# Kernel optimization log

Hardware: AMD Instinct MI355X
Metric: run time of the kernel (lower is better)

Reference implementation:

```python
import jax, jax.numpy as jnp
import numpy as np
from jax import lax

N, C, H, W = 8, 512, 28, 28
G = 8                     # attention groups
QKP = 32                  # qk_planes = out/groups/2
VP = 64                   # v_planes = branch/groups
BP = 512                  # branch_planes
HW = H * W
EPS = 1e-5                # BatchNorm eps (eval mode, running_mean=0, running_var=1)


def bn(x, gamma, beta, axis=1):
    shape = [1] * x.ndim
    shape[axis] = x.shape[axis]
    g = gamma.reshape(shape)
    b = beta.reshape(shape)
    return x * (g / jnp.sqrt(1.0 + EPS)) + b


def conv2d(x, w, groups=1):
    return lax.conv_general_dilated(
        x, w, (1, 1), 'SAME',
        dimension_numbers=('NCHW', 'OIHW', 'NCHW'),
        feature_group_count=groups)


def setup_inputs() -> dict:
    key = jax.random.key(0)
    ks = jax.random.split(key, 16)
    pe_dim = 2 * QKP + VP  # 128
    inp = {
        'x':        jax.random.normal(ks[0], (N, C, H, W), jnp.float32),
        'qkv_w':    jax.random.normal(ks[1], (BP * 2, C), jnp.float32) * np.sqrt(1.0 / C),
        'g_qkv':    jax.random.normal(ks[2], (BP * 2,), jnp.float32) * 0.1 + 1.0,
        'b_qkv':    jax.random.normal(ks[3], (BP * 2,), jnp.float32) * 0.1,
        'g_sim':    jax.random.normal(ks[4], (G * 3,), jnp.float32) * 0.1 + 1.0,
        'b_sim':    jax.random.normal(ks[5], (G * 3,), jnp.float32) * 0.1,
        'g_out':    jax.random.normal(ks[6], (BP * 2,), jnp.float32) * 0.1 + 1.0,
        'b_out':    jax.random.normal(ks[7], (BP * 2,), jnp.float32) * 0.1,
        'relative': jax.random.normal(ks[8], (pe_dim, 2 * HW - 1), jnp.float32) * np.sqrt(1.0 / VP),
        'xw1':      jax.random.normal(ks[9], (BP, C // G, 3, 3), jnp.float32) * np.sqrt(2.0 / (C // G * 9)),
        'xw2':      jax.random.normal(ks[10], (BP, BP, 1, 1), jnp.float32) * np.sqrt(2.0 / BP),
        'g_x':      jnp.ones((BP,), jnp.float32),
        'b_x':      jnp.zeros((BP,), jnp.float32),
        'rw':       jax.random.normal(ks[11], (BP, BP * 2, 1, 1), jnp.float32) * np.sqrt(2.0 / (BP * 2)),
        'g_r':      jnp.ones((BP,), jnp.float32),
        'b_r':      jnp.zeros((BP,), jnp.float32),
        'pw':       jax.random.normal(ks[12], (BP, BP, 1, 1), jnp.float32) * np.sqrt(2.0 / BP),
        'g_p':      jnp.ones((BP,), jnp.float32),
        'b_p':      jnp.zeros((BP,), jnp.float32),
    }
    return inp


def reference(x, qkv_w, g_qkv, b_qkv, g_sim, b_sim, g_out, b_out, relative,
              xw1, xw2, g_x, b_x, rw, g_r, b_r, pw, g_p, b_p):
    n = x.shape[0]
    # ---- unary branch: grouped 3x3 conv + 1x1 conv + BN ----
    unary = conv2d(x, xw1, groups=G)
    unary = conv2d(unary, xw2)
    unary = bn(unary, g_x, b_x)

    # ---- binary branch (attention over HW tokens) ----
    xf = x.reshape(n, C, HW)
    qkv = jnp.einsum('oc,bci->boi', qkv_w, xf)          # Conv1d k=1
    qkv = bn(qkv, g_qkv, b_qkv)
    qkv = qkv.reshape(n, G, 2 * QKP + VP, HW)
    q = qkv[:, :, :QKP]
    k = qkv[:, :, QKP:2 * QKP]
    v = qkv[:, :, 2 * QKP:]

    # relative position embeddings via index gather: emb[c,i,j] = relative[c, i-j+HW-1]
    idx = jnp.arange(HW)
    rel_idx = idx[:, None] - idx[None, :] + HW - 1      # [HW, HW]
    emb = relative[:, rel_idx]                           # [pe_dim, HW, HW]
    q_emb, k_emb, v_emb = emb[:QKP], emb[QKP:2 * QKP], emb[2 * QKP:]

    qk = jnp.einsum('bgci,bgcj->bgij', q, k)
    qr = jnp.einsum('bgci,cij->bgij', q, q_emb)
    kr = jnp.einsum('bgci,cij->bgij', k, k_emb).swapaxes(2, 3)
    stacked = jnp.concatenate([qk, qr, kr], axis=1)      # [n, 3G, HW, HW]
    stacked = bn(stacked, g_sim, b_sim)
    logits = stacked.reshape(n, 3, G, HW, HW).sum(axis=1)
    sim = jax.nn.softmax(logits, axis=-1)                # softmax over keys j

    sv = jnp.einsum('bgij,bgcj->bgci', sim, v)
    sve = jnp.einsum('bgij,cij->bgci', sim, v_emb)
    stacked_binary = jnp.concatenate([sv, sve], axis=-1).reshape(n, BP * 2, HW)
    stacked_binary = bn(stacked_binary, g_out, b_out)
    binary = stacked_binary.reshape(n, BP, 2, HW).sum(axis=2).reshape(n, BP, H, W)

    # ---- gating / reasoning path ----
    gate_in = jnp.concatenate([unary, binary], axis=1)   # [n, 2*BP, H, W]
    r = jax.nn.relu(gate_in)
    r = jax.nn.relu(bn(conv2d(r, rw), g_r, b_r))
    gate = jax.nn.sigmoid(bn(conv2d(r, pw), g_p, b_p))

    return gate * binary + unary


if __name__ == '__main__':
    out = reference(**setup_inputs())
    print(out.shape, out.dtype)
```

## Files before the change

kernel.cpp:

```cpp
#include <hip/hip_runtime.h>
#include <math.h>


typedef unsigned short u16;
typedef unsigned int u32;
typedef __bf16 bf16x8 __attribute__((ext_vector_type(8)));
typedef float f32x4 __attribute__((ext_vector_type(4)));

#define INVS 0.99999500003749968f
#define MFMA16(a, b, c) __builtin_amdgcn_mfma_f32_16x16x32_bf16(a, b, c, 0, 0, 0)

__device__ inline u16 f2bf(float f) {
  u32 u = __builtin_bit_cast(u32, f);
  return (u16)((u + 0x7fffu + ((u >> 16) & 1u)) >> 16);
}
__device__ inline bf16x8 ld_bf8(const u16* p) {
  int4 v = *reinterpret_cast<const int4*>(p);
  return __builtin_bit_cast(bf16x8, v);
}
__device__ inline bf16x8 pack8(const u16 h[8]) {
  int4 v;
  v.x = (int)((u32)h[0] | ((u32)h[1] << 16));
  v.y = (int)((u32)h[2] | ((u32)h[3] << 16));
  v.z = (int)((u32)h[4] | ((u32)h[5] << 16));
  v.w = (int)((u32)h[6] | ((u32)h[7] << 16));
  return __builtin_bit_cast(bf16x8, v);
}
__device__ inline bf16x8 zero8() {
  int4 z = {0, 0, 0, 0};
  return __builtin_bit_cast(bf16x8, z);
}
__device__ inline float bpermf(float v, int srcl) {
  return __builtin_bit_cast(float,
      __builtin_amdgcn_ds_bpermute(srcl << 2, __builtin_bit_cast(int, v)));
}

__global__ __launch_bounds__(256) void k_prep(
    const float* __restrict__ qkv_w, const float* __restrict__ xw2,
    const float* __restrict__ rw, const float* __restrict__ pw,
    const float* __restrict__ xw1, const float* __restrict__ rel,
    u16* __restrict__ Wq, u16* __restrict__ W2, u16* __restrict__ Wr,
    u16* __restrict__ Wp, u16* __restrict__ W1t, u16* __restrict__ relq,
    u16* __restrict__ relk, u16* __restrict__ relv) {
  int idx = blockIdx.x * 256 + threadIdx.x;
  if (idx < 524288) { Wq[idx] = f2bf(qkv_w[idx]); return; }
  idx -= 524288;
  if (idx < 262144) { W2[idx] = f2bf(xw2[idx]); return; }
  idx -= 262144;
  if (idx < 524288) { Wr[idx] = f2bf(rw[idx]); return; }
  idx -= 524288;
  if (idx < 262144) { Wp[idx] = f2bf(pw[idx]); return; }
  idx -= 262144;
  if (idx < 294912) {
    int gk = idx >> 12, rem = idx & 4095, oc = rem >> 6, ic = rem & 63;
    int g = gk / 9, k9 = gk % 9;
    W1t[idx] = f2bf(xw1[(((g * 64 + oc) * 64) + ic) * 9 + k9]);
    return;
  }
  idx -= 294912;
  if (idx < 51200) {
    int t = idx >> 5, c = idx & 31;
    relq[idx] = (t < 1567) ? f2bf(rel[c * 1567 + t]) : (u16)0;
    return;
  }
  idx -= 51200;
  if (idx < 51200) {
    int t = idx >> 5, c = idx & 31;
    relk[idx] = (t < 1567) ? f2bf(rel[(32 + c) * 1567 + t]) : (u16)0;
    return;
  }
  idx -= 51200;
  if (idx < 102400) {
    int c = idx / 1600, t = idx % 1600;
    relv[idx] = (t < 1567) ? f2bf(rel[(64 + c) * 1567 + t]) : (u16)0;
    return;
  }
}

__global__ __launch_bounds__(256) void k_transpose(const float* __restrict__ x,
                                                   u16* __restrict__ xT) {
  const int b = blockIdx.z, c0 = blockIdx.y * 64, n0 = blockIdx.x * 32;
  const int tid = threadIdx.x;
  __shared__ __align__(16) u16 tl[64][36];
#pragma unroll
  for (int h = 0; h < 2; ++h) {
    int cl = (tid >> 3) + h * 32;
    int n4 = (tid & 7) * 4;
    float4 v = {0.f, 0.f, 0.f, 0.f};
    if (n0 + n4 + 3 < 784)
      v = *reinterpret_cast<const float4*>(x + ((size_t)b * 512 + c0 + cl) * 784 + n0 + n4);
    u32 lo = (u32)f2bf(v.x) | ((u32)f2bf(v.y) << 16);
    u32 hi = (u32)f2bf(v.z) | ((u32)f2bf(v.w) << 16);
    *reinterpret_cast<int2*>(&tl[cl][n4]) = make_int2((int)lo, (int)hi);
  }
  __syncthreads();
  int nl = tid >> 3, c8 = (tid & 7) * 8;
  if (n0 + nl < 784) {
    u16 h[8];
#pragma unroll
    for (int e = 0; e < 8; ++e) h[e] = tl[c8 + e][nl];
    *reinterpret_cast<int4*>(xT + ((size_t)b * 784 + n0 + nl) * 512 + c0 + c8) =
        __builtin_bit_cast(int4, pack8(h));
  }
}

__global__ __launch_bounds__(256) void k_gemm_qkv(
    const u16* __restrict__ W, const u16* __restrict__ xT,
    const float* __restrict__ gq, const float* __restrict__ bq,
    u16* __restrict__ Qs, u16* __restrict__ Ks, u16* __restrict__ Vs) {
  const int b = blockIdx.z, mt = blockIdx.y, n0 = blockIdx.x * 112;
  const int tid = threadIdx.x, lane = tid & 63, wave = tid >> 6;
  const int lm = lane & 15, lq = lane >> 4;
  __shared__ __align__(16) u16 Bl[112 * 40];
  f32x4 zf = {0.f, 0.f, 0.f, 0.f};
  f32x4 acc[7];
#pragma unroll
  for (int t = 0; t < 7; ++t) acc[t] = zf;
  const u16* Bb = xT + ((size_t)b * 784 + n0) * 512;
  const u16* Ar = W + (size_t)(mt * 64 + wave * 16 + lm) * 512;
  const int row0 = tid >> 2, seg8 = (tid & 3) * 8;
  const u16* src0 = Bb + (size_t)row0 * 512 + seg8;
  const u16* src1 = src0 + (size_t)64 * 512;
  u16* dst0 = &Bl[row0 * 40 + seg8];
  u16* dst1 = &Bl[(row0 + 64) * 40 + seg8];
  int4 p0 = *reinterpret_cast<const int4*>(src0);
  int4 p1;
  if (tid < 192) p1 = *reinterpret_cast<const int4*>(src1);
  bf16x8 afc = ld_bf8(Ar + lq * 8);
  for (int ks = 0; ks < 16; ++ks) {
    *reinterpret_cast<int4*>(dst0) = p0;
    if (tid < 192) *reinterpret_cast<int4*>(dst1) = p1;
    __syncthreads();
    bf16x8 af = afc;
    if (ks < 15) {
      p0 = *reinterpret_cast<const int4*>(src0 + (ks + 1) * 32);
      if (tid < 192) p1 = *reinterpret_cast<const int4*>(src1 + (ks + 1) * 32);
      afc = ld_bf8(Ar + (ks + 1) * 32 + lq * 8);
    }
#pragma unroll
    for (int t = 0; t < 7; ++t) {
      bf16x8 bf8 = ld_bf8(&Bl[(t * 16 + lm) * 40 + lq * 8]);
      acc[t] = MFMA16(af, bf8, acc[t]);
    }
    __syncthreads();
  }
  const int og = mt * 64 + wave * 16 + lq * 4;
  float sc[4], bi[4];
#pragma unroll
  for (int r = 0; r < 4; ++r) { sc[r] = gq[og + r] * INVS; bi[r] = bq[og + r]; }
  const int g = og >> 7, r128 = og & 127;
  const size_t bg = (size_t)b * 8 + g;
#pragma unroll
  for (int t = 0; t < 7; ++t) {
    int j = n0 + t * 16 + lm;
    u16 h[4];
#pragma unroll
    for (int r = 0; r < 4; ++r) h[r] = f2bf(acc[t][r] * sc[r] + bi[r]);
    if (r128 < 64) {
      u16* dst = (r128 < 32) ? Qs : Ks;
      int c = r128 & 31;
      u32 lo = (u32)h[0] | ((u32)h[1] << 16);
      u32 hi = (u32)h[2] | ((u32)h[3] << 16);
      *reinterpret_cast<int2*>(dst + (bg * 784 + j) * 32 + c) = make_int2((int)lo, (int)hi);
    } else {
      int c = r128 - 64;
#pragma unroll
      for (int r = 0; r < 4; ++r) Vs[(bg * 64 + c + r) * 784 + j] = h[r];
    }
  }
}

__global__ __launch_bounds__(256) void k_conv1(const u16* __restrict__ xT,
                                               const u16* __restrict__ W1t,
                                               u16* __restrict__ umid) {
  const int b = blockIdx.z, g = blockIdx.y, n0 = blockIdx.x * 112;
  const int tid = threadIdx.x, lane = tid & 63, wave = tid >> 6;
  const int lm = lane & 15, lq = lane >> 4;
  __shared__ __align__(16) u16 xl[170 * 72];
  for (int u = tid; u < 1360; u += 256) {
    int row = u >> 3, seg = u & 7;
    int ng = n0 - 29 + row;
    int4 v = {0, 0, 0, 0};
    if (ng >= 0 && ng < 784)
      v = *reinterpret_cast<const int4*>(xT + ((size_t)b * 784 + ng) * 512 + g * 64 + seg * 8);
    *reinterpret_cast<int4*>(&xl[row * 72 + seg * 8]) = v;
  }
  __syncthreads();
  f32x4 zf = {0.f, 0.f, 0.f, 0.f};
  f32x4 acc[7];
#pragma unroll
  for (int t = 0; t < 7; ++t) acc[t] = zf;
  const u16* Wg = W1t + (size_t)g * 9 * 4096;
#pragma unroll
  for (int k9 = 0; k9 < 9; ++k9) {
    const int dh = k9 / 3 - 1, dw = k9 % 3 - 1;
#pragma unroll
    for (int ks = 0; ks < 2; ++ks) {
      bf16x8 af = ld_bf8(Wg + (k9 * 64 + wave * 16 + lm) * 64 + ks * 32 + lq * 8);
#pragma unroll
      for (int t = 0; t < 7; ++t) {
        int n = n0 + t * 16 + lm;
        int ww = n % 28 + dw;
        bf16x8 bf8;
        if (ww >= 0 && ww < 28)
          bf8 = ld_bf8(&xl[(t * 16 + lm + dh * 28 + dw + 29) * 72 + ks * 32 + lq * 8]);
        else
          bf8 = zero8();
        acc[t] = MFMA16(af, bf8, acc[t]);
      }
    }
  }
  const int oc4 = g * 64 + wave * 16 + lq * 4;
#pragma unroll
  for (int t = 0; t < 7; ++t) {
    int j = n0 + t * 16 + lm;
    u16 h[4];
#pragma unroll
    for (int r = 0; r < 4; ++r) h[r] = f2bf(acc[t][r]);
    u32 lo = (u32)h[0] | ((u32)h[1] << 16);
    u32 hi = (u32)h[2] | ((u32)h[3] << 16);
    *reinterpret_cast<int2*>(umid + ((size_t)b * 784 + j) * 512 + oc4) = make_int2((int)lo, (int)hi);
  }
}

__global__ __launch_bounds__(256) void k_gemm_x2(
    const u16* __restrict__ W, const u16* __restrict__ Bsrc,
    const float* __restrict__ gv, const float* __restrict__ bv,
    float* __restrict__ outT) {
  const int b = blockIdx.z, mt = blockIdx.y, n0 = blockIdx.x * 112;
  const int tid = threadIdx.x, lane = tid & 63, wave = tid >> 6;
  const int lm = lane & 15, lq = lane >> 4;
  __shared__ __align__(16) u16 Bl[112 * 40];
  f32x4 zf = {0.f, 0.f, 0.f, 0.f};
  f32x4 acc[7];
#pragma unroll
  for (int t = 0; t < 7; ++t) acc[t] = zf;
  const u16* Bb = Bsrc + ((size_t)b * 784 + n0) * 512;
  const u16* Ar = W + (size_t)(mt * 64 + wave * 16 + lm) * 512;
  const int row0 = tid >> 2, seg8 = (tid & 3) * 8;
  const u16* src0 = Bb + (size_t)row0 * 512 + seg8;
  const u16* src1 = src0 + (size_t)64 * 512;
  u16* dst0 = &Bl[row0 * 40 + seg8];
  u16* dst1 = &Bl[(row0 + 64) * 40 + seg8];
  int4 p0 = *reinterpret_cast<const int4*>(src0);
  int4 p1;
  if (tid < 192) p1 = *reinterpret_cast<const int4*>(src1);
  bf16x8 afc = ld_bf8(Ar + lq * 8);
  for (int ks = 0; ks < 16; ++ks) {
    *reinterpret_cast<int4*>(dst0) = p0;
    if (tid < 192) *reinterpret_cast<int4*>(dst1) = p1;
    __syncthreads();
    bf16x8 af = afc;
    if (ks < 15) {
      p0 = *reinterpret_cast<const int4*>(src0 + (ks + 1) * 32);
      if (tid < 192) p1 = *reinterpret_cast<const int4*>(src1 + (ks + 1) * 32);
      afc = ld_bf8(Ar + (ks + 1) * 32 + lq * 8);
    }
#pragma unroll
    for (int t = 0; t < 7; ++t) {
      bf16x8 bf8 = ld_bf8(&Bl[(t * 16 + lm) * 40 + lq * 8]);
      acc[t] = MFMA16(af, bf8, acc[t]);
    }
    __syncthreads();
  }
  const int og = mt * 64 + wave * 16 + lq * 4;
  float sc[4], bi[4];
#pragma unroll
  for (int r = 0; r < 4; ++r) { sc[r] = gv[og + r] * INVS; bi[r] = bv[og + r]; }
#pragma unroll
  for (int t = 0; t < 7; ++t) {
    int j = n0 + t * 16 + lm;
    float4 o4;
    o4.x = acc[t][0] * sc[0] + bi[0];
    o4.y = acc[t][1] * sc[1] + bi[1];
    o4.z = acc[t][2] * sc[2] + bi[2];
    o4.w = acc[t][3] * sc[3] + bi[3];
    *reinterpret_cast<float4*>(outT + ((size_t)b * 784 + j) * 512 + og) = o4;
  }
}

__global__ __launch_bounds__(256) void k_attn(
    const u16* __restrict__ Qs, const u16* __restrict__ Ks, const u16* __restrict__ Vs,
    const u16* __restrict__ relq, const u16* __restrict__ relk, const u16* __restrict__ relv,
    const float* __restrict__ g_sim, const float* __restrict__ g_out,
    const float* __restrict__ b_out, float* __restrict__ binT) {
  const int b = blockIdx.z, g = blockIdx.y, i0 = blockIdx.x * 16;
  const int tid = threadIdx.x, lane = tid & 63, wave = tid >> 6;
  const int lm = lane & 15, lq = lane >> 4;
  __shared__ __align__(16) u16 Pl[16 + 16 * 872];
  __shared__ __align__(16) float KRs[4][16][34];
  __shared__ float WM[4][16];
  __shared__ float rstat[16];
  for (int u = tid; u < 1424; u += 256) {
    int idx = (u < 16) ? u : (16 + ((u - 16) / 88) * 872 + 784 + (u - 16) % 88);
    Pl[idx] = 0;
  }
  const float s0 = g_sim[g] * INVS, s1 = g_sim[8 + g] * INVS, s2 = g_sim[16 + g] * INVS;
  const size_t bg = (size_t)b * 8 + g;
  const u16* Qb = Qs + bg * 784 * 32;
  const u16* Kb = Ks + bg * 784 * 32;
  const u16* Vb = Vs + bg * 64 * 784;
  const bf16x8 aq = ld_bf8(Qb + (i0 + lm) * 32 + lq * 8);
  const f32x4 zf = {0.f, 0.f, 0.f, 0.f};
  float vmax[4] = {-1e30f, -1e30f, -1e30f, -1e30f};
  bf16x8 kfc, bq0c, bq1c, bk0c, bk1c;
  {
    const int j0 = wave * 16;
    const int d0 = 768 + i0 - j0, e0 = 768 + j0 - i0;
    kfc = ld_bf8(Kb + (j0 + lm) * 32 + lq * 8);
    bq0c = ld_bf8(relq + (d0 + lm) * 32 + lq * 8);
    bq1c = ld_bf8(relq + (d0 + 16 + lm) * 32 + lq * 8);
    bk0c = ld_bf8(relk + (e0 + lm) * 32 + lq * 8);
    bk1c = ld_bf8(relk + (e0 + 16 + lm) * 32 + lq * 8);
  }
  int jt = wave;
  for (int rr = 0; rr < 13; ++rr) {
    const int jtn = jt + 4;
    bf16x8 kfn = kfc, bq0n = bq0c, bq1n = bq1c, bk0n = bk0c, bk1n = bk1c;
    if (jtn < 49) {
      const int j0n = jtn * 16;
      const int d0 = 768 + i0 - j0n, e0 = 768 + j0n - i0;
      kfn = ld_bf8(Kb + (j0n + lm) * 32 + lq * 8);
      bq0n = ld_bf8(relq + (d0 + lm) * 32 + lq * 8);
      bq1n = ld_bf8(relq + (d0 + 16 + lm) * 32 + lq * 8);
      bk0n = ld_bf8(relk + (e0 + lm) * 32 + lq * 8);
      bk1n = ld_bf8(relk + (e0 + 16 + lm) * 32 + lq * 8);
    }
    if (jt < 49) {
      const int j0 = jt * 16;
      f32x4 aqk = MFMA16(aq, kfc, zf);
      f32x4 q0 = MFMA16(aq, bq0c, zf);
      f32x4 q1 = MFMA16(aq, bq1c, zf);
      f32x4 k0 = MFMA16(kfc, bk0c, zf);
      f32x4 k1 = MFMA16(kfc, bk1c, zf);
#pragma unroll
      for (int r = 0; r < 4; ++r) {
        int m = lq * 4 + r;
        KRs[wave][m][lm] = k0[r];
        KRs[wave][m][16 + lm] = k1[r];
      }
#pragma unroll
      for (int r = 0; r < 4; ++r) {
        int m = lq * 4 + r, n = lm;
        int c = m - n + 15;
        int srcl = (c & 15) | (lane & 48);
        float t0 = bpermf(q0[r], srcl), t1 = bpermf(q1[r], srcl);
        float qv = (c & 16) ? t1 : t0;
        float kv = KRs[wave][n][n - m + 15];
        float val = aqk[r] * s0 + qv * s1 + kv * s2;
        vmax[r] = fmaxf(vmax[r], val);
        _Float16 hv = (_Float16)val;
        Pl[16 + m * 872 + j0 + n] = __builtin_bit_cast(u16, hv);
      }
    }
    jt = jtn;
    kfc = kfn; bq0c = bq0n; bq1c = bq1n; bk0c = bk0n; bk1c = bk1n;
  }
#pragma unroll
  for (int r = 0; r < 4; ++r) {
#pragma unroll
    for (int d = 1; d < 16; d <<= 1) vmax[r] = fmaxf(vmax[r], __shfl_xor(vmax[r], d, 64));
  }
  if (lm == 0) {
#pragma unroll
    for (int r = 0; r < 4; ++r) WM[wave][lq * 4 + r] = vmax[r];
  }
  __syncthreads();
  {
    const int row = tid >> 4, sub = tid & 15;
    u16* Pr = &Pl[16 + row * 872];
    float gmax = fmaxf(fmaxf(WM[0][row], WM[1][row]), fmaxf(WM[2][row], WM[3][row]));
    float sm = 0.f;
    for (int k = 0; k < 49; ++k) {
      int j = sub + 16 * k;
      _Float16 hv = __builtin_bit_cast(_Float16, Pr[j]);
      float e = __expf((float)hv - gmax);
      sm += e;
      Pr[j] = f2bf(e);
    }
#pragma unroll
    for (int d = 1; d < 16; d <<= 1) sm += __shfl_xor(sm, d, 64);
    if (sub == 0) rstat[row] = 1.0f / sm;
  }
  __syncthreads();
  f32x4 accV = zf, accE = zf;
  const int coff = wave * 16;
  const u16* Vr = Vb + (size_t)(coff + lm) * 784;
  const u16* Rr = relv + (size_t)(coff + lm) * 1600 + i0;
  const u16* Prow = &Pl[16 + lm * 872];
  for (int ks = 0; ks < 25; ++ks) {
    bf16x8 ap = ld_bf8(Prow + ks * 32 + lq * 8);
    bf16x8 bv = ld_bf8(Vr + ks * 32 + lq * 8);
    accV = MFMA16(ap, bv, accV);
    const int base = 783 + lm - ks * 32 - lq * 8;
    u16 h[8];
#pragma unroll
    for (int e = 0; e < 8; ++e) h[e] = Prow[base - e];
    bf16x8 ash = pack8(h);
    bf16x8 br = ld_bf8(Rr + ks * 32 + lq * 8);
    accE = MFMA16(ash, br, accE);
  }
  const int c = coff + lm;
  const int oi = g * 128 + 2 * c;
  const float so0 = g_out[oi] * INVS, bo0 = b_out[oi];
  const float so1 = g_out[oi + 1] * INVS, bo1 = b_out[oi + 1];
#pragma unroll
  for (int r = 0; r < 4; ++r) {
    int row = lq * 4 + r;
    float rl = rstat[row];
    float val = accV[r] * rl * so0 + bo0 + accE[r] * rl * so1 + bo1;
    binT[((size_t)b * 784 + i0 + row) * 512 + g * 64 + c] = val;
  }
}

__global__ __launch_bounds__(256) void k_gemm_rw(
    const u16* __restrict__ W, const float* __restrict__ unT, const float* __restrict__ binT,
    const float* __restrict__ gv, const float* __restrict__ bv, u16* __restrict__ rT) {
  const int b = blockIdx.z, mt = blockIdx.y, n0 = blockIdx.x * 112;
  const int tid = threadIdx.x, lane = tid & 63, wave = tid >> 6;
  const int lm = lane & 15, lq = lane >> 4;
  __shared__ __align__(16) u16 Bl[112 * 40];
  f32x4 zf = {0.f, 0.f, 0.f, 0.f};
  f32x4 acc[7];
#pragma unroll
  for (int t = 0; t < 7; ++t) acc[t] = zf;
  const u16* Ar = W + (size_t)(mt * 64 + wave * 16 + lm) * 1024;
  const int row0 = tid >> 2, seg8 = (tid & 3) * 8;
  const size_t off0 = ((size_t)b * 784 + n0 + row0) * 512 + seg8;
  const size_t off1 = off0 + (size_t)64 * 512;
  u16* dst0 = &Bl[row0 * 40 + seg8];
  u16* dst1 = &Bl[(row0 + 64) * 40 + seg8];
  auto ldrow = [](const float* sp, float4& a, float4& b) {
    a = *reinterpret_cast<const float4*>(sp);
    b = *reinterpret_cast<const float4*>(sp + 4);
  };
  auto cvt_store = [](u16* dst, float4 a, float4 b) {
    u16 h[8] = {f2bf(fmaxf(a.x, 0.f)), f2bf(fmaxf(a.y, 0.f)),
                f2bf(fmaxf(a.z, 0.f)), f2bf(fmaxf(a.w, 0.f)),
                f2bf(fmaxf(b.x, 0.f)), f2bf(fmaxf(b.y, 0.f)),
                f2bf(fmaxf(b.z, 0.f)), f2bf(fmaxf(b.w, 0.f))};
    *reinterpret_cast<int4*>(dst) = __builtin_bit_cast(int4, pack8(h));
  };
  float4 a0, b0, a1, b1;
  ldrow(unT + off0, a0, b0);
  if (tid < 192) ldrow(unT + off1, a1, b1);
  bf16x8 afc = ld_bf8(Ar + lq * 8);
  for (int ks = 0; ks < 32; ++ks) {
    cvt_store(dst0, a0, b0);
    if (tid < 192) cvt_store(dst1, a1, b1);
    __syncthreads();
    bf16x8 af = afc;
    if (ks < 31) {
      const int ksn = ks + 1;
      const float* sb = (ksn < 16) ? unT : binT;
      const int k0 = (ksn & 15) * 32;
      ldrow(sb + off0 + k0, a0, b0);
      if (tid < 192) ldrow(sb + off1 + k0, a1, b1);
      afc = ld_bf8(Ar + ksn * 32 + lq * 8);
    }
#pragma unroll
    for (int t = 0; t < 7; ++t) {
      bf16x8 bf8 = ld_bf8(&Bl[(t * 16 + lm) * 40 + lq * 8]);
      acc[t] = MFMA16(af, bf8, acc[t]);
    }
    __syncthreads();
  }
  const int og = mt * 64 + wave * 16 + lq * 4;
  float sc[4], bi[4];
#pragma unroll
  for (int r = 0; r < 4; ++r) { sc[r] = gv[og + r] * INVS; bi[r] = bv[og + r]; }
#pragma unroll
  for (int t = 0; t < 7; ++t) {
    int j = n0 + t * 16 + lm;
    u16 h[4];
#pragma unroll
    for (int r = 0; r < 4; ++r) h[r] = f2bf(fmaxf(acc[t][r] * sc[r] + bi[r], 0.f));
    u32 lo = (u32)h[0] | ((u32)h[1] << 16);
    u32 hi = (u32)h[2] | ((u32)h[3] << 16);
    *reinterpret_cast<int2*>(rT + ((size_t)b * 784 + j) * 512 + og) = make_int2((int)lo, (int)hi);
  }
}

__global__ __launch_bounds__(256) void k_gemm_pw(
    const u16* __restrict__ W, const u16* __restrict__ rT,
    const float* __restrict__ gv, const float* __restrict__ bv,
    const float* __restrict__ binT, const float* __restrict__ unT,
    float* __restrict__ out) {
  const int b = blockIdx.z, mt = blockIdx.y, n0 = blockIdx.x * 112;
  const int tid = threadIdx.x, lane = tid & 63, wave = tid >> 6;
  const int lm = lane & 15, lq = lane >> 4;
  __shared__ __align__(16) u16 Bl[112 * 40];
  f32x4 zf = {0.f, 0.f, 0.f, 0.f};
  f32x4 acc[7];
#pragma unroll
  for (int t = 0; t < 7; ++t) acc[t] = zf;
  const u16* Bb = rT + ((size_t)b * 784 + n0) * 512;
  const u16* Ar = W + (size_t)(mt * 64 + wave * 16 + lm) * 512;
  const int row0 = tid >> 2, seg8 = (tid & 3) * 8;
  const u16* src0 = Bb + (size_t)row0 * 512 + seg8;
  const u16* src1 = src0 + (size_t)64 * 512;
  u16* dst0 = &Bl[row0 * 40 + seg8];
  u16* dst1 = &Bl[(row0 + 64) * 40 + seg8];
  int4 p0 = *reinterpret_cast<const int4*>(src0);
  int4 p1;
  if (tid < 192) p1 = *reinterpret_cast<const int4*>(src1);
  bf16x8 afc = ld_bf8(Ar + lq * 8);
  for (int ks = 0; ks < 16; ++ks) {
    *reinterpret_cast<int4*>(dst0) = p0;
    if (tid < 192) *reinterpret_cast<int4*>(dst1) = p1;
    __syncthreads();
    bf16x8 af = afc;
    if (ks < 15) {
      p0 = *reinterpret_cast<const int4*>(src0 + (ks + 1) * 32);
      if (tid < 192) p1 = *reinterpret_cast<const int4*>(src1 + (ks + 1) * 32);
      afc = ld_bf8(Ar + (ks + 1) * 32 + lq * 8);
    }
#pragma unroll
    for (int t = 0; t < 7; ++t) {
      bf16x8 bf8 = ld_bf8(&Bl[(t * 16 + lm) * 40 + lq * 8]);
      acc[t] = MFMA16(af, bf8, acc[t]);
    }
    __syncthreads();
  }
  const int og = mt * 64 + wave * 16 + lq * 4;
  float sc[4], bi[4];
#pragma unroll
  for (int r = 0; r < 4; ++r) { sc[r] = gv[og + r] * INVS; bi[r] = bv[og + r]; }
#pragma unroll
  for (int t = 0; t < 7; ++t) {
    int j = n0 + t * 16 + lm;
    float4 bin4 = *reinterpret_cast<const float4*>(binT + ((size_t)b * 784 + j) * 512 + og);
    float4 un4 = *reinterpret_cast<const float4*>(unT + ((size_t)b * 784 + j) * 512 + og);
    float binv[4] = {bin4.x, bin4.y, bin4.z, bin4.w};
    float unv[4] = {un4.x, un4.y, un4.z, un4.w};
#pragma unroll
    for (int r = 0; r < 4; ++r) {
      float gt = 1.f / (1.f + __expf(-(acc[t][r] * sc[r] + bi[r])));
      out[((size_t)b * 512 + og + r) * 784 + j] = gt * binv[r] + unv[r];
    }
  }
}

extern "C" void kernel_launch(void* const* d_in, const int* in_sizes, int n_in,
                              void* d_out, int out_size, void* d_ws, size_t ws_size,
                              hipStream_t stream) {
  const float* x = (const float*)d_in[0];
  const float* qkv_w = (const float*)d_in[1];
  const float* g_qkv = (const float*)d_in[2];
  const float* b_qkv = (const float*)d_in[3];
  const float* g_sim = (const float*)d_in[4];
  const float* g_out = (const float*)d_in[6];
  const float* b_out = (const float*)d_in[7];
  const float* relative = (const float*)d_in[8];
  const float* xw1 = (const float*)d_in[9];
  const float* xw2 = (const float*)d_in[10];
  const float* g_x = (const float*)d_in[11];
  const float* b_x = (const float*)d_in[12];
  const float* rw = (const float*)d_in[13];
  const float* g_r = (const float*)d_in[14];
  const float* b_r = (const float*)d_in[15];
  const float* pw = (const float*)d_in[16];
  const float* g_p = (const float*)d_in[17];
  const float* b_p = (const float*)d_in[18];

  char* p = (char*)d_ws;
  auto take = [&](size_t n) { char* q = p; p += (n + 255) & ~(size_t)255; return q; };
  u16* xT = (u16*)take((size_t)8 * 784 * 512 * 2);
  u16* Wq = (u16*)take((size_t)1024 * 512 * 2);
  u16* W2 = (u16*)take((size_t)512 * 512 * 2);
  u16* Wr = (u16*)take((size_t)512 * 1024 * 2);
  u16* Wp = (u16*)take((size_t)512 * 512 * 2);
  u16* W1t = (u16*)take((size_t)294912 * 2);
  u16* relq = (u16*)take((size_t)51200 * 2);
  u16* relk = (u16*)take((size_t)51200 * 2);
  u16* relv = (u16*)take((size_t)102400 * 2);
  u16* Qs = (u16*)take((size_t)8 * 8 * 784 * 32 * 2);
  u16* Ks = (u16*)take((size_t)8 * 8 * 784 * 32 * 2);
  u16* Vs = (u16*)take(((size_t)8 * 8 * 64 * 784 + 64) * 2);
  u16* umid = (u16*)take((size_t)8 * 784 * 512 * 2);
  float* unT = (float*)take((size_t)8 * 784 * 512 * 4);
  float* binT = (float*)take((size_t)8 * 784 * 512 * 4);
  u16* rT = (u16*)take((size_t)8 * 784 * 512 * 2);

  k_prep<<<dim3(8096), dim3(256), 0, stream>>>(qkv_w, xw2, rw, pw, xw1, relative,
                                               Wq, W2, Wr, Wp, W1t, relq, relk, relv);
  k_transpose<<<dim3(25, 8, 8), dim3(256), 0, stream>>>(x, xT);
  k_gemm_qkv<<<dim3(7, 16, 8), dim3(256), 0, stream>>>(Wq, xT, g_qkv, b_qkv, Qs, Ks, Vs);
  k_conv1<<<dim3(7, 8, 8), dim3(256), 0, stream>>>(xT, W1t, umid);
  k_gemm_x2<<<dim3(7, 8, 8), dim3(256), 0, stream>>>(W2, umid, g_x, b_x, unT);
  k_attn<<<dim3(49, 8, 8), dim3(256), 0, stream>>>(Qs, Ks, Vs, relq, relk, relv,
                                                   g_sim, g_out, b_out, binT);
  k_gemm_rw<<<dim3(7, 8, 8), dim3(256), 0, stream>>>(Wr, unT, binT, g_r, b_r, rT);
  k_gemm_pw<<<dim3(7, 8, 8), dim3(256), 0, stream>>>(Wp, rT, g_p, b_p, binT, unT,
                                                     (float*)d_out);
}
```

Measured before the change: 301.0 us.

## Merge independent kernels into combined launches with block-index dispatch

Independent stages are paired into single launches: transpose with weight prep, conv1 with the QKV GEMM, and the x2 GEMM with attention. Each pair shares a flat grid, and the block index selects which body runs. This cuts the kernel count from eight to five and lets independent work fill the GPU together, reducing launch gaps and tail idle time. The cost is that each merged kernel's shared memory is sized for the larger body (up to about 37KB), which may lower occupancy for the lighter blocks.

```diff
diff --git a/kernel.cpp b/kernel.cpp
--- a/kernel.cpp
+++ b/kernel.cpp
@@ -35,14 +35,14 @@
       __builtin_amdgcn_ds_bpermute(srcl << 2, __builtin_bit_cast(int, v)));
 }
 
-__global__ __launch_bounds__(256) void k_prep(
-    const float* __restrict__ qkv_w, const float* __restrict__ xw2,
+
+__device__ void body_prep(
+    int idx, const float* __restrict__ qkv_w, const float* __restrict__ xw2,
     const float* __restrict__ rw, const float* __restrict__ pw,
     const float* __restrict__ xw1, const float* __restrict__ rel,
     u16* __restrict__ Wq, u16* __restrict__ W2, u16* __restrict__ Wr,
     u16* __restrict__ Wp, u16* __restrict__ W1t, u16* __restrict__ relq,
     u16* __restrict__ relk, u16* __restrict__ relv) {
-  int idx = blockIdx.x * 256 + threadIdx.x;
   if (idx < 524288) { Wq[idx] = f2bf(qkv_w[idx]); return; }
   idx -= 524288;
   if (idx < 262144) { W2[idx] = f2bf(xw2[idx]); return; }
@@ -77,11 +77,11 @@
   }
 }
 
-__global__ __launch_bounds__(256) void k_transpose(const float* __restrict__ x,
-                                                   u16* __restrict__ xT) {
-  const int b = blockIdx.z, c0 = blockIdx.y * 64, n0 = blockIdx.x * 32;
+__device__ void body_transpose(int bx, int by, int bz, const float* __restrict__ x,
+                               u16* __restrict__ xT, char* smem) {
+  const int b = bz, c0 = by * 64, n0 = bx * 32;
   const int tid = threadIdx.x;
-  __shared__ __align__(16) u16 tl[64][36];
+  u16(*tl)[36] = reinterpret_cast<u16(*)[36]>(smem);
 #pragma unroll
   for (int h = 0; h < 2; ++h) {
     int cl = (tid >> 3) + h * 32;
@@ -104,14 +104,15 @@
   }
 }
 
-__global__ __launch_bounds__(256) void k_gemm_qkv(
-    const u16* __restrict__ W, const u16* __restrict__ xT,
-    const float* __restrict__ gq, const float* __restrict__ bq,
-    u16* __restrict__ Qs, u16* __restrict__ Ks, u16* __restrict__ Vs) {
-  const int b = blockIdx.z, mt = blockIdx.y, n0 = blockIdx.x * 112;
+__device__ void body_qkv(int bx, int by, int bz,
+                         const u16* __restrict__ W, const u16* __restrict__ xT,
+                         const float* __restrict__ gq, const float* __restrict__ bq,
+                         u16* __restrict__ Qs, u16* __restrict__ Ks,
+                         u16* __restrict__ Vs, char* smem) {
+  const int b = bz, mt = by, n0 = bx * 112;
   const int tid = threadIdx.x, lane = tid & 63, wave = tid >> 6;
   const int lm = lane & 15, lq = lane >> 4;
-  __shared__ __align__(16) u16 Bl[112 * 40];
+  u16* Bl = reinterpret_cast<u16*>(smem);
   f32x4 zf = {0.f, 0.f, 0.f, 0.f};
   f32x4 acc[7];
 #pragma unroll
@@ -170,13 +171,13 @@
   }
 }
 
-__global__ __launch_bounds__(256) void k_conv1(const u16* __restrict__ xT,
-                                               const u16* __restrict__ W1t,
-                                               u16* __restrict__ umid) {
-  const int b = blockIdx.z, g = blockIdx.y, n0 = blockIdx.x * 112;
+__device__ void body_conv1(int bx, int by, int bz, const u16* __restrict__ xT,
+                           const u16* __restrict__ W1t, u16* __restrict__ umid,
+                           char* smem) {
+  const int b = bz, g = by, n0 = bx * 112;
   const int tid = threadIdx.x, lane = tid & 63, wave = tid >> 6;
   const int lm = lane & 15, lq = lane >> 4;
-  __shared__ __align__(16) u16 xl[170 * 72];
+  u16* xl = reinterpret_cast<u16*>(smem);
   for (int u = tid; u < 1360; u += 256) {
     int row = u >> 3, seg = u & 7;
     int ng = n0 - 29 + row;
@@ -223,14 +224,14 @@
   }
 }
 
-__global__ __launch_bounds__(256) void k_gemm_x2(
-    const u16* __restrict__ W, const u16* __restrict__ Bsrc,
-    const float* __restrict__ gv, const float* __restrict__ bv,
-    float* __restrict__ outT) {
-  const int b = blockIdx.z, mt = blockIdx.y, n0 = blockIdx.x * 112;
+__device__ void body_x2(int bx, int by, int bz,
+                        const u16* __restrict__ W, const u16* __restrict__ Bsrc,
+                        const float* __restrict__ gv, const float* __restrict__ bv,
+                        float* __restrict__ outT, char* smem) {
+  const int b = bz, mt = by, n0 = bx * 112;
   const int tid = threadIdx.x, lane = tid & 63, wave = tid >> 6;
   const int lm = lane & 15, lq = lane >> 4;
-  __shared__ __align__(16) u16 Bl[112 * 40];
+  u16* Bl = reinterpret_cast<u16*>(smem);
   f32x4 zf = {0.f, 0.f, 0.f, 0.f};
   f32x4 acc[7];
 #pragma unroll
@@ -279,18 +280,20 @@
   }
 }
 
-__global__ __launch_bounds__(256) void k_attn(
-    const u16* __restrict__ Qs, const u16* __restrict__ Ks, const u16* __restrict__ Vs,
-    const u16* __restrict__ relq, const u16* __restrict__ relk, const u16* __restrict__ relv,
-    const float* __restrict__ g_sim, const float* __restrict__ g_out,
-    const float* __restrict__ b_out, float* __restrict__ binT) {
-  const int b = blockIdx.z, g = blockIdx.y, i0 = blockIdx.x * 16;
+__device__ void body_attn(int bx, int by, int bz,
+                          const u16* __restrict__ Qs, const u16* __restrict__ Ks,
+                          const u16* __restrict__ Vs, const u16* __restrict__ relq,
+                          const u16* __restrict__ relk, const u16* __restrict__ relv,
+                          const float* __restrict__ g_sim, const float* __restrict__ g_out,
+                          const float* __restrict__ b_out, float* __restrict__ binT,
+                          char* smem) {
+  const int b = bz, g = by, i0 = bx * 16;
   const int tid = threadIdx.x, lane = tid & 63, wave = tid >> 6;
   const int lm = lane & 15, lq = lane >> 4;
-  __shared__ __align__(16) u16 Pl[16 + 16 * 872];
-  __shared__ __align__(16) float KRs[4][16][34];
-  __shared__ float WM[4][16];
-  __shared__ float rstat[16];
+  u16* Pl = reinterpret_cast<u16*>(smem);
+  float* KRs = reinterpret_cast<float*>(smem + 27936);
+  float* WM = reinterpret_cast<float*>(smem + 36640);
+  float* rstat = reinterpret_cast<float*>(smem + 36896);
   for (int u = tid; u < 1424; u += 256) {
     int idx = (u < 16) ? u : (16 + ((u - 16) / 88) * 872 + 784 + (u - 16) % 88);
     Pl[idx] = 0;
@@ -336,8 +339,8 @@
 #pragma unroll
       for (int r = 0; r < 4; ++r) {
         int m = lq * 4 + r;
-        KRs[wave][m][lm] = k0[r];
-        KRs[wave][m][16 + lm] = k1[r];
+        KRs[(wave * 16 + m) * 34 + lm] = k0[r];
+        KRs[(wave * 16 + m) * 34 + 16 + lm] = k1[r];
       }
 #pragma unroll
       for (int r = 0; r < 4; ++r) {
@@ -346,7 +349,7 @@
         int srcl = (c & 15) | (lane & 48);
         float t0 = bpermf(q0[r], srcl), t1 = bpermf(q1[r], srcl);
         float qv = (c & 16) ? t1 : t0;
-        float kv = KRs[wave][n][n - m + 15];
+        float kv = KRs[(wave * 16 + n) * 34 + (n - m + 15)];
         float val = aqk[r] * s0 + qv * s1 + kv * s2;
         vmax[r] = fmaxf(vmax[r], val);
         _Float16 hv = (_Float16)val;
@@ -363,13 +366,13 @@
   }
   if (lm == 0) {
 #pragma unroll
-    for (int r = 0; r < 4; ++r) WM[wave][lq * 4 + r] = vmax[r];
+    for (int r = 0; r < 4; ++r) WM[wave * 16 + lq * 4 + r] = vmax[r];
   }
   __syncthreads();
   {
     const int row = tid >> 4, sub = tid & 15;
     u16* Pr = &Pl[16 + row * 872];
-    float gmax = fmaxf(fmaxf(WM[0][row], WM[1][row]), fmaxf(WM[2][row], WM[3][row]));
+    float gmax = fmaxf(fmaxf(WM[row], WM[16 + row]), fmaxf(WM[32 + row], WM[48 + row]));
     float sm = 0.f;
     for (int k = 0; k < 49; ++k) {
       int j = sub + 16 * k;
@@ -410,6 +413,60 @@
     float rl = rstat[row];
     float val = accV[r] * rl * so0 + bo0 + accE[r] * rl * so1 + bo1;
     binT[((size_t)b * 784 + i0 + row) * 512 + g * 64 + c] = val;
+  }
+}
+
+
+__global__ __launch_bounds__(256) void k_pt(
+    const float* __restrict__ x, u16* __restrict__ xT,
+    const float* __restrict__ qkv_w, const float* __restrict__ xw2,
+    const float* __restrict__ rw, const float* __restrict__ pw,
+    const float* __restrict__ xw1, const float* __restrict__ rel,
+    u16* __restrict__ Wq, u16* __restrict__ W2, u16* __restrict__ Wr,
+    u16* __restrict__ Wp, u16* __restrict__ W1t, u16* __restrict__ relq,
+    u16* __restrict__ relk, u16* __restrict__ relv) {
+  __shared__ __align__(16) char smem[4608];
+  const int bid = blockIdx.x;
+  if (bid < 1600) {
+    body_transpose(bid % 25, (bid / 25) % 8, bid / 200, x, xT, smem);
+  } else {
+    body_prep((bid - 1600) * 256 + threadIdx.x, qkv_w, xw2, rw, pw, xw1, rel,
+              Wq, W2, Wr, Wp, W1t, relq, relk, relv);
+  }
+}
+
+__global__ __launch_bounds__(256) void k_qc(
+    const u16* __restrict__ Wq, const u16* __restrict__ xT,
+    const float* __restrict__ gq, const float* __restrict__ bq,
+    u16* __restrict__ Qs, u16* __restrict__ Ks, u16* __restrict__ Vs,
+    const u16* __restrict__ W1t, u16* __restrict__ umid) {
+  __shared__ __align__(16) char smem[24480];
+  const int bid = blockIdx.x;
+  if (bid < 448) {
+    body_conv1(bid % 7, (bid / 7) % 8, bid / 56, xT, W1t, umid, smem);
+  } else {
+    const int q = bid - 448;
+    body_qkv(q % 7, (q / 7) % 16, q / 112, Wq, xT, gq, bq, Qs, Ks, Vs, smem);
+  }
+}
+
+__global__ __launch_bounds__(256) void k_ax(
+    const u16* __restrict__ W2, const u16* __restrict__ umid,
+    const float* __restrict__ g_x, const float* __restrict__ b_x,
+    float* __restrict__ unT,
+    const u16* __restrict__ Qs, const u16* __restrict__ Ks, const u16* __restrict__ Vs,
+    const u16* __restrict__ relq, const u16* __restrict__ relk,
+    const u16* __restrict__ relv, const float* __restrict__ g_sim,
+    const float* __restrict__ g_out, const float* __restrict__ b_out,
+    float* __restrict__ binT) {
+  __shared__ __align__(16) char smem[36960];
+  const int bid = blockIdx.x;
+  if (bid < 448) {
+    body_x2(bid % 7, (bid / 7) % 8, bid / 56, W2, umid, g_x, b_x, unT, smem);
+  } else {
+    const int a = bid - 448;
+    body_attn(a % 49, (a / 49) % 8, a / 392, Qs, Ks, Vs, relq, relk, relv,
+              g_sim, g_out, b_out, binT, smem);
   }
 }
 
@@ -582,14 +639,11 @@
   float* binT = (float*)take((size_t)8 * 784 * 512 * 4);
   u16* rT = (u16*)take((size_t)8 * 784 * 512 * 2);
 
-  k_prep<<<dim3(8096), dim3(256), 0, stream>>>(qkv_w, xw2, rw, pw, xw1, relative,
-                                               Wq, W2, Wr, Wp, W1t, relq, relk, relv);
-  k_transpose<<<dim3(25, 8, 8), dim3(256), 0, stream>>>(x, xT);
-  k_gemm_qkv<<<dim3(7, 16, 8), dim3(256), 0, stream>>>(Wq, xT, g_qkv, b_qkv, Qs, Ks, Vs);
-  k_conv1<<<dim3(7, 8, 8), dim3(256), 0, stream>>>(xT, W1t, umid);
-  k_gemm_x2<<<dim3(7, 8, 8), dim3(256), 0, stream>>>(W2, umid, g_x, b_x, unT);
-  k_attn<<<dim3(49, 8, 8), dim3(256), 0, stream>>>(Qs, Ks, Vs, relq, relk, relv,
-                                                   g_sim, g_out, b_out, binT);
+  k_pt<<<dim3(9696), dim3(256), 0, stream>>>(x, xT, qkv_w, xw2, rw, pw, xw1, relative,
+                                             Wq, W2, Wr, Wp, W1t, relq, relk, relv);
+  k_qc<<<dim3(1344), dim3(256), 0, stream>>>(Wq, xT, g_qkv, b_qkv, Qs, Ks, Vs, W1t, umid);
+  k_ax<<<dim3(3584), dim3(256), 0, stream>>>(W2, umid, g_x, b_x, unT, Qs, Ks, Vs,
+                                             relq, relk, relv, g_sim, g_out, b_out, binT);
   k_gemm_rw<<<dim3(7, 8, 8), dim3(256), 0, stream>>>(Wr, unT, binT, g_r, b_r, rT);
   k_gemm_pw<<<dim3(7, 8, 8), dim3(256), 0, stream>>>(Wp, rT, g_p, b_p, binT, unT,
                                                      (float*)d_out);
```

After: 299.2 us. No clear change (-0.6%).
